# Performance work log

Hardware: AMD Instinct MI355X
Metric: run time of the kernel (lower is better)

The kernel has to match this reference:

```python
import jax, jax.numpy as jnp
import numpy as np

N_USERS = 100000
N_ITEMS = 50000
N_TOPICS = 1000
N_NODES = N_USERS + N_ITEMS + N_TOPICS
DIM = 64
LAYERS = 3
NNZ = 4000000
BATCH = 16384


def setup_inputs() -> dict:
    key = jax.random.key(0)
    ks = jax.random.split(key, 8)
    user_w = jax.random.normal(ks[0], (N_USERS, DIM), dtype=jnp.float32) * 0.1
    item_w = jax.random.normal(ks[1], (N_ITEMS, DIM), dtype=jnp.float32) * 0.1
    topic_w = jax.random.normal(ks[2], (N_TOPICS, DIM), dtype=jnp.float32) * 0.1
    vals = jax.random.uniform(ks[3], (NNZ,), dtype=jnp.float32)
    row = jax.random.randint(ks[4], (NNZ,), 0, N_NODES, dtype=jnp.int32)
    col = jax.random.randint(ks[5], (NNZ,), 0, N_NODES, dtype=jnp.int32)
    users = jax.random.randint(ks[6], (BATCH,), 0, N_USERS, dtype=jnp.int32)
    items = jax.random.randint(ks[7], (BATCH,), 0, N_ITEMS, dtype=jnp.int32)
    return {"user_w": user_w, "item_w": item_w, "topic_w": topic_w,
            "vals": vals, "row": row, "col": col,
            "users": users, "items": items}


def _spmm(vals, row, col, x):
    # y[r] = sum over edges e with row[e]==r of vals[e] * x[col[e]]
    msgs = vals[:, None] * x[col]  # [NNZ, DIM]
    return jax.ops.segment_sum(msgs, row, num_segments=N_NODES)


def reference(user_w, item_w, topic_w, vals, row, col, users, items):
    all_emb = jnp.concatenate([user_w, item_w, topic_w], axis=0)  # [N, D]
    acc = all_emb
    emb = all_emb
    for _ in range(LAYERS):
        emb = _spmm(vals, row, col, emb)
        acc = acc + emb
    out = acc / jnp.asarray(LAYERS + 1, dtype=acc.dtype)  # mean over stacked layers
    u = out[users]                       # [B, D] user rows
    i = out[N_USERS + items]             # [B, D] item rows (offset into node table)
    return jnp.sum(u * i, axis=1)        # [B]
```

## Files before the change

kernel.cpp:

```cpp
#include <hip/hip_runtime.h>
#include <hip/hip_fp16.h>

#define N_USERS 100000
#define N_ITEMS 50000
#define N_TOPICS 1000
#define N_NODES (N_USERS + N_ITEMS + N_TOPICS)
#define DIM 64
#define NNZ 4000000
#define BATCH 16384

#define BROWS 128
#define NB ((N_NODES + BROWS - 1) / BROWS)
#define NPART 256
#define CHUNK ((NNZ + NPART - 1) / NPART)
#define SEGCAP 4608

#define QSCALE 16384.0f
#define QINV   6.103515625e-05f

__global__ void concat_init(const float4* __restrict__ uw,
                            const float4* __restrict__ iw,
                            const float4* __restrict__ tw,
                            __half2* __restrict__ x0) {
    int tid = blockIdx.x * blockDim.x + threadIdx.x;
    const int total = N_NODES * (DIM / 4);
    if (tid >= total) return;
    int node = tid >> 4;
    int q = tid & 15;
    float4 v;
    if (node < N_USERS)                v = uw[node * 16 + q];
    else if (node < N_USERS + N_ITEMS) v = iw[(node - N_USERS) * 16 + q];
    else                               v = tw[(node - N_USERS - N_ITEMS) * 16 + q];
    x0[tid * 2]     = __floats2half2_rn(v.x, v.y);
    x0[tid * 2 + 1] = __floats2half2_rn(v.z, v.w);
}

__global__ void __launch_bounds__(1024)
part_count(const int* __restrict__ row, int* __restrict__ hcnt) {
    __shared__ int h[NB];
    const int g = blockIdx.x;
    const int t = threadIdx.x;
    for (int i = t; i < NB; i += 1024) h[i] = 0;
    __syncthreads();
    int e0 = g * CHUNK;
    int e1 = e0 + CHUNK; if (e1 > NNZ) e1 = NNZ;
    for (int e = e0 + t; e < e1; e += 1024) {
        int r = __builtin_nontemporal_load(&row[e]);
        atomicAdd(&h[r >> 7], 1);
    }
    __syncthreads();
    int* dst = hcnt + (size_t)g * NB;
    for (int i = t; i < NB; i += 1024) dst[i] = h[i];
}

__global__ void part_scanA(int* __restrict__ hcnt, int* __restrict__ bcnt) {
    int b = blockIdx.x * 4 + (threadIdx.x >> 6);
    int lane = threadIdx.x & 63;
    if (b >= NB) return;
    int carry = 0;
    for (int base = 0; base < NPART; base += 64) {
        int g = base + lane;
        int v = hcnt[(size_t)g * NB + b];
        int x = v;
        #pragma unroll
        for (int off = 1; off < 64; off <<= 1) {
            int y = __shfl_up(x, off, 64);
            if (lane >= off) x += y;
        }
        int tot = __shfl(x, 63, 64);
        hcnt[(size_t)g * NB + b] = carry + x - v;
        carry += tot;
    }
    if (lane == 0) bcnt[b] = carry;
}

__global__ void part_scanB(const int* __restrict__ bcnt,
                           int* __restrict__ bptr,
                           int* __restrict__ rowptr) {
    __shared__ int wsum[16];
    __shared__ int carry_s;
    const int t = threadIdx.x;
    const int lane = t & 63;
    const int wid = t >> 6;
    if (t == 0) carry_s = 0;
    __syncthreads();
    for (int base = 0; base < NB; base += 1024) {
        int i = base + t;
        int v = (i < NB) ? bcnt[i] : 0;
        int x = v;
        #pragma unroll
        for (int off = 1; off < 64; off <<= 1) {
            int y = __shfl_up(x, off, 64);
            if (lane >= off) x += y;
        }
        if (lane == 63) wsum[wid] = x;
        __syncthreads();
        int wbase = 0;
        for (int w = 0; w < wid; ++w) wbase += wsum[w];
        int excl = carry_s + wbase + (x - v);
        if (i < NB) bptr[i] = excl;
        __syncthreads();
        if (t == 1023) carry_s = excl + v;
        __syncthreads();
    }
    if (t == 0) { bptr[NB] = NNZ; rowptr[N_NODES] = NNZ; }
}

__global__ void __launch_bounds__(1024)
part_scatter(const int* __restrict__ row,
             const int* __restrict__ col,
             const float* __restrict__ vals,
             const int* __restrict__ hcnt,
             const int* __restrict__ bptr,
             int2* __restrict__ cvtmp) {
    __shared__ int cur[NB];
    const int g = blockIdx.x;
    const int t = threadIdx.x;
    const int* hoff = hcnt + (size_t)g * NB;
    for (int i = t; i < NB; i += 1024) cur[i] = bptr[i] + hoff[i];
    __syncthreads();
    int e0 = g * CHUNK;
    int e1 = e0 + CHUNK; if (e1 > NNZ) e1 = NNZ;
    for (int e = e0 + t; e < e1; e += 1024) {
        int r = __builtin_nontemporal_load(&row[e]);
        int c = __builtin_nontemporal_load(&col[e]);
        float v = __builtin_nontemporal_load(&vals[e]);
        int p = atomicAdd(&cur[r >> 7], 1);
        cvtmp[p] = make_int2(((r & (BROWS - 1)) << 18) | c, __float_as_int(v));
    }
}

__global__ void __launch_bounds__(256)
bucket_sort(const int* __restrict__ bptr,
            const long long* __restrict__ cvtmp,
            unsigned int* __restrict__ cv,
            int* __restrict__ rowptr) {
    __shared__ int2 seg[SEGCAP];
    __shared__ int cnt[BROWS];
    __shared__ int cur[BROWS];
    const int t = threadIdx.x;
    const int b = blockIdx.x;
    const int beg = bptr[b];
    const int end = bptr[b + 1];
    const int n = end - beg;

    for (int i = t; i < BROWS; i += 256) cnt[i] = 0;
    const bool lds_path = (n <= SEGCAP);

    if (lds_path) {
        for (int j = t; j < n; j += 256) {
            long long e = __builtin_nontemporal_load(&cvtmp[beg + j]);
            seg[j] = make_int2((int)e, (int)(e >> 32));
        }
    }
    __syncthreads();

    if (lds_path) {
        for (int j = t; j < n; j += 256)
            atomicAdd(&cnt[(seg[j].x >> 18) & (BROWS - 1)], 1);
    } else {
        for (int j = beg + t; j < end; j += 256) {
            long long e = cvtmp[j];
            atomicAdd(&cnt[((int)e >> 18) & (BROWS - 1)], 1);
        }
    }
    __syncthreads();

    if (t < 64) {
        int lane = t;
        int v0 = cnt[lane];
        int v1 = cnt[64 + lane];
        int x0 = v0;
        #pragma unroll
        for (int off = 1; off < 64; off <<= 1) {
            int y = __shfl_up(x0, off, 64);
            if (lane >= off) x0 += y;
        }
        int tot0 = __shfl(x0, 63, 64);
        int x1 = v1;
        #pragma unroll
        for (int off = 1; off < 64; off <<= 1) {
            int y = __shfl_up(x1, off, 64);
            if (lane >= off) x1 += y;
        }
        x1 += tot0;
        int e0 = x0 - v0;
        int e1 = x1 - v1;
        cur[lane] = e0;
        cur[64 + lane] = e1;
        int rowbase = b * BROWS;
        if (rowbase + lane < N_NODES)      rowptr[rowbase + lane] = beg + e0;
        if (rowbase + 64 + lane < N_NODES) rowptr[rowbase + 64 + lane] = beg + e1;
    }
    __syncthreads();

    if (lds_path) {
        for (int j = t; j < n; j += 256) {
            int2 e = seg[j];
            int p = atomicAdd(&cur[(e.x >> 18) & (BROWS - 1)], 1);
            float v = __int_as_float(e.y);
            unsigned int qv = (unsigned int)(v * QSCALE + 0.5f);
            if (qv > 16383u) qv = 16383u;
            cv[beg + p] = (qv << 18) | (unsigned int)(e.x & 0x3FFFF);
        }
    } else {
        for (int j = beg + t; j < end; j += 256) {
            long long e = cvtmp[j];
            int lo = (int)e;
            float v = __int_as_float((int)(e >> 32));
            int p = atomicAdd(&cur[(lo >> 18) & (BROWS - 1)], 1);
            unsigned int qv = (unsigned int)(v * QSCALE + 0.5f);
            if (qv > 16383u) qv = 16383u;
            cv[beg + p] = (qv << 18) | (unsigned int)(lo & 0x3FFFF);
        }
    }
}

__global__ void spmm_csr(const int* __restrict__ rowptr,
                         const unsigned int* __restrict__ cv,
                         const __half2* __restrict__ x2,
                         __half2* __restrict__ y2) {
    int blk = blockIdx.x;
    int bucket = (blk >> 8) * 8 + (blk & 7);
    int sub = (blk & 255) >> 3;
    int r = bucket * BROWS + sub * 4 + (threadIdx.x >> 6);
    if (r >= N_NODES) return;
    int lane = threadIdx.x & 63;
    int half = lane >> 5;
    int d = lane & 31;
    int beg = rowptr[r];
    int end = rowptr[r + 1];
    float ax0 = 0.0f, ay0 = 0.0f, ax1 = 0.0f, ay1 = 0.0f;
    int j = beg + half;
    for (; j + 14 < end; j += 16) {
        unsigned int u[8];
        __half2 h[8];
        #pragma unroll
        for (int k = 0; k < 8; ++k) u[k] = cv[j + 2 * k];
        #pragma unroll
        for (int k = 0; k < 8; ++k) h[k] = x2[(size_t)(u[k] & 0x3FFFF) * 32 + d];
        #pragma unroll
        for (int k = 0; k < 8; k += 2) {
            float2 f0 = __half22float2(h[k]);
            float2 f1 = __half22float2(h[k + 1]);
            float v0 = (float)(u[k] >> 18) * QINV;
            float v1 = (float)(u[k + 1] >> 18) * QINV;
            ax0 = fmaf(v0, f0.x, ax0); ay0 = fmaf(v0, f0.y, ay0);
            ax1 = fmaf(v1, f1.x, ax1); ay1 = fmaf(v1, f1.y, ay1);
        }
    }
    for (; j + 6 < end; j += 8) {
        unsigned int u0 = cv[j];
        unsigned int u1 = cv[j + 2];
        unsigned int u2 = cv[j + 4];
        unsigned int u3 = cv[j + 6];
        float2 f0 = __half22float2(x2[(size_t)(u0 & 0x3FFFF) * 32 + d]);
        float2 f1 = __half22float2(x2[(size_t)(u1 & 0x3FFFF) * 32 + d]);
        float2 f2 = __half22float2(x2[(size_t)(u2 & 0x3FFFF) * 32 + d]);
        float2 f3 = __half22float2(x2[(size_t)(u3 & 0x3FFFF) * 32 + d]);
        float v0 = (float)(u0 >> 18) * QINV;
        float v1 = (float)(u1 >> 18) * QINV;
        float v2 = (float)(u2 >> 18) * QINV;
        float v3 = (float)(u3 >> 18) * QINV;
        ax0 = fmaf(v0, f0.x, ax0); ay0 = fmaf(v0, f0.y, ay0);
        ax1 = fmaf(v1, f1.x, ax1); ay1 = fmaf(v1, f1.y, ay1);
        ax0 = fmaf(v2, f2.x, ax0); ay0 = fmaf(v2, f2.y, ay0);
        ax1 = fmaf(v3, f3.x, ax1); ay1 = fmaf(v3, f3.y, ay1);
    }
    for (; j < end; j += 2) {
        unsigned int u = cv[j];
        float2 f = __half22float2(x2[(size_t)(u & 0x3FFFF) * 32 + d]);
        float v = (float)(u >> 18) * QINV;
        ax0 = fmaf(v, f.x, ax0); ay0 = fmaf(v, f.y, ay0);
    }
    float ax = ax0 + ax1;
    float ay = ay0 + ay1;
    ax += __shfl_down(ax, 32, 64);
    ay += __shfl_down(ay, 32, 64);
    if (lane < 32) {
        __half2 o = __floats2half2_rn(ax, ay);
        unsigned int ob;
        __builtin_memcpy(&ob, &o, 4);
        __builtin_nontemporal_store(ob, (unsigned int*)&y2[(size_t)r * 32 + d]);
    }
}

__global__ void spmm_batch(const int* __restrict__ rowptr,
                           const unsigned int* __restrict__ cv,
                           const __half2* __restrict__ x2,
                           const int* __restrict__ users,
                           const int* __restrict__ items,
                           float* __restrict__ accb) {
    int b = blockIdx.x * 4 + (threadIdx.x >> 6);
    if (b >= 2 * BATCH) return;
    int lane = threadIdx.x & 63;
    int half = lane >> 5;
    int d = lane & 31;
    int r = (b < BATCH) ? users[b] : (N_USERS + items[b - BATCH]);
    int beg = rowptr[r];
    int end = rowptr[r + 1];
    float ax0 = 0.0f, ay0 = 0.0f, ax1 = 0.0f, ay1 = 0.0f;
    int j = beg + half;
    for (; j + 14 < end; j += 16) {
        unsigned int u[8];
        __half2 h[8];
        #pragma unroll
        for (int k = 0; k < 8; ++k) u[k] = cv[j + 2 * k];
        #pragma unroll
        for (int k = 0; k < 8; ++k) h[k] = x2[(size_t)(u[k] & 0x3FFFF) * 32 + d];
        #pragma unroll
        for (int k = 0; k < 8; k += 2) {
            float2 f0 = __half22float2(h[k]);
            float2 f1 = __half22float2(h[k + 1]);
            float v0 = (float)(u[k] >> 18) * QINV;
            float v1 = (float)(u[k + 1] >> 18) * QINV;
            ax0 = fmaf(v0, f0.x, ax0); ay0 = fmaf(v0, f0.y, ay0);
            ax1 = fmaf(v1, f1.x, ax1); ay1 = fmaf(v1, f1.y, ay1);
        }
    }
    for (; j + 6 < end; j += 8) {
        unsigned int u0 = cv[j];
        unsigned int u1 = cv[j + 2];
        unsigned int u2 = cv[j + 4];
        unsigned int u3 = cv[j + 6];
        float2 f0 = __half22float2(x2[(size_t)(u0 & 0x3FFFF) * 32 + d]);
        float2 f1 = __half22float2(x2[(size_t)(u1 & 0x3FFFF) * 32 + d]);
        float2 f2 = __half22float2(x2[(size_t)(u2 & 0x3FFFF) * 32 + d]);
        float2 f3 = __half22float2(x2[(size_t)(u3 & 0x3FFFF) * 32 + d]);
        float v0 = (float)(u0 >> 18) * QINV;
        float v1 = (float)(u1 >> 18) * QINV;
        float v2 = (float)(u2 >> 18) * QINV;
        float v3 = (float)(u3 >> 18) * QINV;
        ax0 = fmaf(v0, f0.x, ax0); ay0 = fmaf(v0, f0.y, ay0);
        ax1 = fmaf(v1, f1.x, ax1); ay1 = fmaf(v1, f1.y, ay1);
        ax0 = fmaf(v2, f2.x, ax0); ay0 = fmaf(v2, f2.y, ay0);
        ax1 = fmaf(v3, f3.x, ax1); ay1 = fmaf(v3, f3.y, ay1);
    }
    for (; j < end; j += 2) {
        unsigned int u = cv[j];
        float2 f = __half22float2(x2[(size_t)(u & 0x3FFFF) * 32 + d]);
        float v = (float)(u >> 18) * QINV;
        ax0 = fmaf(v, f.x, ax0); ay0 = fmaf(v, f.y, ay0);
    }
    float ax = ax0 + ax1;
    float ay = ay0 + ay1;
    ax += __shfl_down(ax, 32, 64);
    ay += __shfl_down(ay, 32, 64);
    if (lane < 32) {
        float2* a2 = (float2*)(accb + (size_t)b * 64 + 2 * d);
        float2 o = *a2;
        o.x += ax; o.y += ay;
        *a2 = o;
    }
}

__global__ void batch_init(const float4* __restrict__ uw,
                           const float4* __restrict__ iw,
                           const int* __restrict__ users,
                           const int* __restrict__ items,
                           float4* __restrict__ accb) {
    int tid = blockIdx.x * blockDim.x + threadIdx.x;
    const int total = 2 * BATCH * (DIM / 4);
    if (tid >= total) return;
    int r = tid >> 4;
    int q = tid & 15;
    float4 v;
    if (r < BATCH) v = uw[(size_t)users[r] * 16 + q];
    else           v = iw[(size_t)items[r - BATCH] * 16 + q];
    accb[tid] = v;
}

__global__ void batch_add(const __half* __restrict__ emb,
                          const int* __restrict__ users,
                          const int* __restrict__ items,
                          float4* __restrict__ accb) {
    int tid = blockIdx.x * blockDim.x + threadIdx.x;
    const int total = 2 * BATCH * (DIM / 4);
    if (tid >= total) return;
    int r = tid >> 4;
    int q = tid & 15;
    int node = (r < BATCH) ? users[r] : (N_USERS + items[r - BATCH]);
    const __half2* e2 = (const __half2*)(emb + (size_t)node * 64 + q * 4);
    float2 lo = __half22float2(e2[0]);
    float2 hi = __half22float2(e2[1]);
    float4 a = accb[tid];
    a.x += lo.x; a.y += lo.y; a.z += hi.x; a.w += hi.y;
    accb[tid] = a;
}

__global__ void final_dot(const float* __restrict__ accb,
                          float* __restrict__ out) {
    int b = blockIdx.x * 4 + (threadIdx.x >> 6);
    int lane = threadIdx.x & 63;
    if (b >= BATCH) return;
    float pu = accb[(size_t)b * 64 + lane];
    float pi = accb[(size_t)(BATCH + b) * 64 + lane];
    float p = pu * pi;
    #pragma unroll
    for (int off = 32; off > 0; off >>= 1)
        p += __shfl_down(p, off, 64);
    if (lane == 0) out[b] = p * (1.0f / 16.0f);
}

extern "C" void kernel_launch(void* const* d_in, const int* in_sizes, int n_in,
                              void* d_out, int out_size, void* d_ws, size_t ws_size,
                              hipStream_t stream) {
    const float* uw   = (const float*)d_in[0];
    const float* iw   = (const float*)d_in[1];
    const float* tw   = (const float*)d_in[2];
    const float* vals = (const float*)d_in[3];
    const int*   row  = (const int*)d_in[4];
    const int*   col  = (const int*)d_in[5];
    const int*   users= (const int*)d_in[6];
    const int*   items= (const int*)d_in[7];
    float* out = (float*)d_out;

    char* ws = (char*)d_ws;
    const size_t NODE_F = (size_t)N_NODES * DIM;
    __half* A     = (__half*)ws; ws += NODE_F * 2;
    __half* B     = (__half*)ws; ws += NODE_F * 2;
    float* ACCB   = (float*)ws;  ws += (size_t)2 * BATCH * DIM * 4;
    int*   bcnt   = (int*)ws;    ws += (size_t)NB * 4;
    int*   bptr   = (int*)ws;    ws += (size_t)(NB + 1) * 4;
    int*   rowptr = (int*)ws;    ws += (size_t)(N_NODES + 1) * 4;
    int*   hcnt   = (int*)ws;    ws += (size_t)NPART * NB * 4;
    unsigned int* cv = (unsigned int*)ws; ws += (size_t)NNZ * 4;
    int2*  cvtmp  = (int2*)ws;   ws += (size_t)NNZ * 8;

    const int node_v4  = N_NODES * (DIM / 4);
    const int batch_v4 = 2 * BATCH * (DIM / 4);

    concat_init<<<(node_v4 + 255) / 256, 256, 0, stream>>>(
        (const float4*)uw, (const float4*)iw, (const float4*)tw, (__half2*)A);
    batch_init<<<(batch_v4 + 255) / 256, 256, 0, stream>>>(
        (const float4*)uw, (const float4*)iw, users, items, (float4*)ACCB);

    part_count<<<NPART, 1024, 0, stream>>>(row, hcnt);
    part_scanA<<<(NB + 3) / 4, 256, 0, stream>>>(hcnt, bcnt);
    part_scanB<<<1, 1024, 0, stream>>>(bcnt, bptr, rowptr);
    part_scatter<<<NPART, 1024, 0, stream>>>(row, col, vals, hcnt, bptr, cvtmp);
    bucket_sort<<<NB, 256, 0, stream>>>(bptr, (const long long*)cvtmp, cv, rowptr);

    const int spmm_blocks = ((NB + 7) / 8) * 256;
    spmm_csr<<<spmm_blocks, 256, 0, stream>>>(rowptr, cv, (const __half2*)A,
                                              (__half2*)B);
    batch_add<<<(batch_v4 + 255) / 256, 256, 0, stream>>>(
        B, users, items, (float4*)ACCB);
    spmm_csr<<<spmm_blocks, 256, 0, stream>>>(rowptr, cv, (const __half2*)B,
                                              (__half2*)A);
    batch_add<<<(batch_v4 + 255) / 256, 256, 0, stream>>>(
        A, users, items, (float4*)ACCB);
    spmm_batch<<<(2 * BATCH + 3) / 4, 256, 0, stream>>>(
        rowptr, cv, (const __half2*)A, users, items, ACCB);

    final_dot<<<(BATCH + 3) / 4, 256, 0, stream>>>(ACCB, out);
}
```

Before: 442.7 us.

## Fuse setup kernels and map one SpMM row per half-wavefront

Merges concat, batch init and partition counting into one launch, and folds the two scan kernels into one using a last-block atomic counter. The SpMM kernels now assign each 32-lane half-wave its own row instead of splitting a row's edges across the two halves. This removes the cross-half shuffle reduction and reduces launch overhead. In exchange, each row's edges are processed serially by one half-wave, which lengthens per-row dependency chains and increases load imbalance on long rows.

```diff
diff --git a/kernel.cpp b/kernel.cpp
--- a/kernel.cpp
+++ b/kernel.cpp
@@ -18,45 +18,71 @@
 #define QSCALE 16384.0f
 #define QINV   6.103515625e-05f
 
-__global__ void concat_init(const float4* __restrict__ uw,
-                            const float4* __restrict__ iw,
-                            const float4* __restrict__ tw,
-                            __half2* __restrict__ x0) {
-    int tid = blockIdx.x * blockDim.x + threadIdx.x;
-    const int total = N_NODES * (DIM / 4);
-    if (tid >= total) return;
-    int node = tid >> 4;
-    int q = tid & 15;
-    float4 v;
-    if (node < N_USERS)                v = uw[node * 16 + q];
-    else if (node < N_USERS + N_ITEMS) v = iw[(node - N_USERS) * 16 + q];
-    else                               v = tw[(node - N_USERS - N_ITEMS) * 16 + q];
-    x0[tid * 2]     = __floats2half2_rn(v.x, v.y);
-    x0[tid * 2 + 1] = __floats2half2_rn(v.z, v.w);
-}
+#define CONCAT_TOTAL (N_NODES * (DIM / 4))
+#define CONCAT_BLOCKS ((CONCAT_TOTAL + 1023) / 1024)
+#define BINIT_TOTAL (2 * BATCH * (DIM / 4))
+#define BINIT_BLOCKS ((BINIT_TOTAL + 1023) / 1024)
 
 __global__ void __launch_bounds__(1024)
-part_count(const int* __restrict__ row, int* __restrict__ hcnt) {
+phase0(const float4* __restrict__ uw,
+       const float4* __restrict__ iw,
+       const float4* __restrict__ tw,
+       const int* __restrict__ row,
+       const int* __restrict__ users,
+       const int* __restrict__ items,
+       __half2* __restrict__ x0,
+       float4* __restrict__ accb,
+       int* __restrict__ hcnt,
+       int* __restrict__ sync) {
     __shared__ int h[NB];
-    const int g = blockIdx.x;
+    const int blk = blockIdx.x;
     const int t = threadIdx.x;
-    for (int i = t; i < NB; i += 1024) h[i] = 0;
-    __syncthreads();
-    int e0 = g * CHUNK;
-    int e1 = e0 + CHUNK; if (e1 > NNZ) e1 = NNZ;
-    for (int e = e0 + t; e < e1; e += 1024) {
-        int r = __builtin_nontemporal_load(&row[e]);
-        atomicAdd(&h[r >> 7], 1);
-    }
-    __syncthreads();
-    int* dst = hcnt + (size_t)g * NB;
-    for (int i = t; i < NB; i += 1024) dst[i] = h[i];
-}
-
-__global__ void part_scanA(int* __restrict__ hcnt, int* __restrict__ bcnt) {
-    int b = blockIdx.x * 4 + (threadIdx.x >> 6);
-    int lane = threadIdx.x & 63;
-    if (b >= NB) return;
+    if (blk < NPART) {
+        if (blk == 0 && t == 0) *sync = 0;
+        for (int i = t; i < NB; i += 1024) h[i] = 0;
+        __syncthreads();
+        int e0 = blk * CHUNK;
+        int e1 = e0 + CHUNK; if (e1 > NNZ) e1 = NNZ;
+        for (int e = e0 + t; e < e1; e += 1024) {
+            int r = __builtin_nontemporal_load(&row[e]);
+            atomicAdd(&h[r >> 7], 1);
+        }
+        __syncthreads();
+        int* dst = hcnt + (size_t)blk * NB;
+        for (int i = t; i < NB; i += 1024) dst[i] = h[i];
+    } else if (blk < NPART + CONCAT_BLOCKS) {
+        int tid = (blk - NPART) * 1024 + t;
+        if (tid >= CONCAT_TOTAL) return;
+        int node = tid >> 4;
+        int q = tid & 15;
+        float4 v;
+        if (node < N_USERS)                v = uw[node * 16 + q];
+        else if (node < N_USERS + N_ITEMS) v = iw[(node - N_USERS) * 16 + q];
+        else                               v = tw[(node - N_USERS - N_ITEMS) * 16 + q];
+        x0[tid * 2]     = __floats2half2_rn(v.x, v.y);
+        x0[tid * 2 + 1] = __floats2half2_rn(v.z, v.w);
+    } else {
+        int tid = (blk - NPART - CONCAT_BLOCKS) * 1024 + t;
+        if (tid >= BINIT_TOTAL) return;
+        int r = tid >> 4;
+        int q = tid & 15;
+        float4 v;
+        if (r < BATCH) v = uw[(size_t)users[r] * 16 + q];
+        else           v = iw[(size_t)items[r - BATCH] * 16 + q];
+        accb[tid] = v;
+    }
+}
+
+__global__ void __launch_bounds__(256)
+part_scanAB(int* __restrict__ hcnt,
+            int* __restrict__ bcnt,
+            int* __restrict__ bptr,
+            int* __restrict__ rowptr,
+            int* __restrict__ sync) {
+    const int t = threadIdx.x;
+    const int lane = t & 63;
+    const int wid = t >> 6;
+    int b = blockIdx.x * 4 + wid;
     int carry = 0;
     for (int base = 0; base < NPART; base += 64) {
         int g = base + lane;
@@ -72,19 +98,18 @@
         carry += tot;
     }
     if (lane == 0) bcnt[b] = carry;
-}
-
-__global__ void part_scanB(const int* __restrict__ bcnt,
-                           int* __restrict__ bptr,
-                           int* __restrict__ rowptr) {
-    __shared__ int wsum[16];
+    __syncthreads();
+    __threadfence();
+    __shared__ int lastFlag;
+    if (t == 0) lastFlag = (atomicAdd(sync, 1) == (int)gridDim.x - 1);
+    __syncthreads();
+    if (!lastFlag) return;
+
+    __shared__ int wsum[4];
     __shared__ int carry_s;
-    const int t = threadIdx.x;
-    const int lane = t & 63;
-    const int wid = t >> 6;
     if (t == 0) carry_s = 0;
     __syncthreads();
-    for (int base = 0; base < NB; base += 1024) {
+    for (int base = 0; base < NB; base += 256) {
         int i = base + t;
         int v = (i < NB) ? bcnt[i] : 0;
         int x = v;
@@ -100,7 +125,7 @@
         int excl = carry_s + wbase + (x - v);
         if (i < NB) bptr[i] = excl;
         __syncthreads();
-        if (t == 1023) carry_s = excl + v;
+        if (t == 255) carry_s = excl + v;
         __syncthreads();
     }
     if (t == 0) { bptr[NB] = NNZ; rowptr[N_NODES] = NNZ; }
@@ -220,69 +245,69 @@
                          const unsigned int* __restrict__ cv,
                          const __half2* __restrict__ x2,
                          __half2* __restrict__ y2) {
-    int blk = blockIdx.x;
-    int bucket = (blk >> 8) * 8 + (blk & 7);
-    int sub = (blk & 255) >> 3;
-    int r = bucket * BROWS + sub * 4 + (threadIdx.x >> 6);
-    if (r >= N_NODES) return;
+    int bucket = blockIdx.x >> 4;
+    int sub = blockIdx.x & 15;
     int lane = threadIdx.x & 63;
     int half = lane >> 5;
+    int r = bucket * BROWS + sub * 8 + (threadIdx.x >> 6) * 2 + half;
+    if (r >= N_NODES) return;
     int d = lane & 31;
     int beg = rowptr[r];
     int end = rowptr[r + 1];
-    float ax0 = 0.0f, ay0 = 0.0f, ax1 = 0.0f, ay1 = 0.0f;
-    int j = beg + half;
-    for (; j + 14 < end; j += 16) {
+    float ax = 0.0f, ay = 0.0f;
+    int j = beg;
+    for (; j + 15 < end; j += 16) {
+        unsigned int u[16];
+        __half2 h[16];
+        #pragma unroll
+        for (int k = 0; k < 16; ++k) u[k] = cv[j + k];
+        #pragma unroll
+        for (int k = 0; k < 16; ++k) h[k] = x2[(size_t)(u[k] & 0x3FFFF) * 32 + d];
+        #pragma unroll
+        for (int k = 0; k < 16; ++k) {
+            float2 f = __half22float2(h[k]);
+            float v = (float)(u[k] >> 18) * QINV;
+            ax = fmaf(v, f.x, ax); ay = fmaf(v, f.y, ay);
+        }
+    }
+    for (; j + 7 < end; j += 8) {
         unsigned int u[8];
         __half2 h[8];
         #pragma unroll
-        for (int k = 0; k < 8; ++k) u[k] = cv[j + 2 * k];
+        for (int k = 0; k < 8; ++k) u[k] = cv[j + k];
         #pragma unroll
         for (int k = 0; k < 8; ++k) h[k] = x2[(size_t)(u[k] & 0x3FFFF) * 32 + d];
         #pragma unroll
-        for (int k = 0; k < 8; k += 2) {
-            float2 f0 = __half22float2(h[k]);
-            float2 f1 = __half22float2(h[k + 1]);
-            float v0 = (float)(u[k] >> 18) * QINV;
-            float v1 = (float)(u[k + 1] >> 18) * QINV;
-            ax0 = fmaf(v0, f0.x, ax0); ay0 = fmaf(v0, f0.y, ay0);
-            ax1 = fmaf(v1, f1.x, ax1); ay1 = fmaf(v1, f1.y, ay1);
-        }
-    }
-    for (; j + 6 < end; j += 8) {
-        unsigned int u0 = cv[j];
-        unsigned int u1 = cv[j + 2];
-        unsigned int u2 = cv[j + 4];
-        unsigned int u3 = cv[j + 6];
-        float2 f0 = __half22float2(x2[(size_t)(u0 & 0x3FFFF) * 32 + d]);
-        float2 f1 = __half22float2(x2[(size_t)(u1 & 0x3FFFF) * 32 + d]);
-        float2 f2 = __half22float2(x2[(size_t)(u2 & 0x3FFFF) * 32 + d]);
-        float2 f3 = __half22float2(x2[(size_t)(u3 & 0x3FFFF) * 32 + d]);
-        float v0 = (float)(u0 >> 18) * QINV;
-        float v1 = (float)(u1 >> 18) * QINV;
-        float v2 = (float)(u2 >> 18) * QINV;
-        float v3 = (float)(u3 >> 18) * QINV;
-        ax0 = fmaf(v0, f0.x, ax0); ay0 = fmaf(v0, f0.y, ay0);
-        ax1 = fmaf(v1, f1.x, ax1); ay1 = fmaf(v1, f1.y, ay1);
-        ax0 = fmaf(v2, f2.x, ax0); ay0 = fmaf(v2, f2.y, ay0);
-        ax1 = fmaf(v3, f3.x, ax1); ay1 = fmaf(v3, f3.y, ay1);
-    }
-    for (; j < end; j += 2) {
+        for (int k = 0; k < 8; ++k) {
+            float2 f = __half22float2(h[k]);
+            float v = (float)(u[k] >> 18) * QINV;
+            ax = fmaf(v, f.x, ax); ay = fmaf(v, f.y, ay);
+        }
+    }
+    for (; j + 3 < end; j += 4) {
+        unsigned int u[4];
+        __half2 h[4];
+        #pragma unroll
+        for (int k = 0; k < 4; ++k) u[k] = cv[j + k];
+        #pragma unroll
+        for (int k = 0; k < 4; ++k) h[k] = x2[(size_t)(u[k] & 0x3FFFF) * 32 + d];
+        #pragma unroll
+        for (int k = 0; k < 4; ++k) {
+            float2 f = __half22float2(h[k]);
+            float v = (float)(u[k] >> 18) * QINV;
+            ax = fmaf(v, f.x, ax); ay = fmaf(v, f.y, ay);
+        }
+    }
+    for (; j < end; ++j) {
         unsigned int u = cv[j];
         float2 f = __half22float2(x2[(size_t)(u & 0x3FFFF) * 32 + d]);
         float v = (float)(u >> 18) * QINV;
-        ax0 = fmaf(v, f.x, ax0); ay0 = fmaf(v, f.y, ay0);
-    }
-    float ax = ax0 + ax1;
-    float ay = ay0 + ay1;
-    ax += __shfl_down(ax, 32, 64);
-    ay += __shfl_down(ay, 32, 64);
-    if (lane < 32) {
-        __half2 o = __floats2half2_rn(ax, ay);
-        unsigned int ob;
-        __builtin_memcpy(&ob, &o, 4);
-        __builtin_nontemporal_store(ob, (unsigned int*)&y2[(size_t)r * 32 + d]);
-    }
+        ax = fmaf(v, f.x, ax); ay = fmaf(v, f.y, ay);
+    }
+    __half2 o = __floats2half2_rn(ax, ay);
+    unsigned int ob;
+    __builtin_memcpy(&ob, &o, 4);
+    __builtin_nontemporal_store(ob, (unsigned int*)&y2[(size_t)r * 32 + d]);
 }
 
 __global__ void spmm_batch(const int* __restrict__ rowptr,
@@ -291,83 +316,68 @@
                            const int* __restrict__ users,
                            const int* __restrict__ items,
                            float* __restrict__ accb) {
-    int b = blockIdx.x * 4 + (threadIdx.x >> 6);
-    if (b >= 2 * BATCH) return;
     int lane = threadIdx.x & 63;
     int half = lane >> 5;
+    int b = blockIdx.x * 8 + (threadIdx.x >> 6) * 2 + half;
+    if (b >= 2 * BATCH) return;
     int d = lane & 31;
     int r = (b < BATCH) ? users[b] : (N_USERS + items[b - BATCH]);
     int beg = rowptr[r];
     int end = rowptr[r + 1];
-    float ax0 = 0.0f, ay0 = 0.0f, ax1 = 0.0f, ay1 = 0.0f;
-    int j = beg + half;
-    for (; j + 14 < end; j += 16) {
+    float ax = 0.0f, ay = 0.0f;
+    int j = beg;
+    for (; j + 15 < end; j += 16) {
+        unsigned int u[16];
+        __half2 h[16];
+        #pragma unroll
+        for (int k = 0; k < 16; ++k) u[k] = cv[j + k];
+        #pragma unroll
+        for (int k = 0; k < 16; ++k) h[k] = x2[(size_t)(u[k] & 0x3FFFF) * 32 + d];
+        #pragma unroll
+        for (int k = 0; k < 16; ++k) {
+            float2 f = __half22float2(h[k]);
+            float v = (float)(u[k] >> 18) * QINV;
+            ax = fmaf(v, f.x, ax); ay = fmaf(v, f.y, ay);
+        }
+    }
+    for (; j + 7 < end; j += 8) {
         unsigned int u[8];
         __half2 h[8];
         #pragma unroll
-        for (int k = 0; k < 8; ++k) u[k] = cv[j + 2 * k];
+        for (int k = 0; k < 8; ++k) u[k] = cv[j + k];
         #pragma unroll
         for (int k = 0; k < 8; ++k) h[k] = x2[(size_t)(u[k] & 0x3FFFF) * 32 + d];
         #pragma unroll
-        for (int k = 0; k < 8; k += 2) {
-            float2 f0 = __half22float2(h[k]);
-            float2 f1 = __half22float2(h[k + 1]);
-            float v0 = (float)(u[k] >> 18) * QINV;
-            float v1 = (float)(u[k + 1] >> 18) * QINV;
-            ax0 = fmaf(v0, f0.x, ax0); ay0 = fmaf(v0, f0.y, ay0);
-            ax1 = fmaf(v1, f1.x, ax1); ay1 = fmaf(v1, f1.y, ay1);
-        }
-    }
-    for (; j + 6 < end; j += 8) {
-        unsigned int u0 = cv[j];
-        unsigned int u1 = cv[j + 2];
-        unsigned int u2 = cv[j + 4];
-        unsigned int u3 = cv[j + 6];
-        float2 f0 = __half22float2(x2[(size_t)(u0 & 0x3FFFF) * 32 + d]);
-        float2 f1 = __half22float2(x2[(size_t)(u1 & 0x3FFFF) * 32 + d]);
-        float2 f2 = __half22float2(x2[(size_t)(u2 & 0x3FFFF) * 32 + d]);
-        float2 f3 = __half22float2(x2[(size_t)(u3 & 0x3FFFF) * 32 + d]);
-        float v0 = (float)(u0 >> 18) * QINV;
-        float v1 = (float)(u1 >> 18) * QINV;
-        float v2 = (float)(u2 >> 18) * QINV;
-        float v3 = (float)(u3 >> 18) * QINV;
-        ax0 = fmaf(v0, f0.x, ax0); ay0 = fmaf(v0, f0.y, ay0);
-        ax1 = fmaf(v1, f1.x, ax1); ay1 = fmaf(v1, f1.y, ay1);
-        ax0 = fmaf(v2, f2.x, ax0); ay0 = fmaf(v2, f2.y, ay0);
-        ax1 = fmaf(v3, f3.x, ax1); ay1 = fmaf(v3, f3.y, ay1);
-    }
-    for (; j < end; j += 2) {
+        for (int k = 0; k < 8; ++k) {
+            float2 f = __half22float2(h[k]);
+            float v = (float)(u[k] >> 18) * QINV;
+            ax = fmaf(v, f.x, ax); ay = fmaf(v, f.y, ay);
+        }
+    }
+    for (; j + 3 < end; j += 4) {
+        unsigned int u[4];
+        __half2 h[4];
+        #pragma unroll
+        for (int k = 0; k < 4; ++k) u[k] = cv[j + k];
+        #pragma unroll
+        for (int k = 0; k < 4; ++k) h[k] = x2[(size_t)(u[k] & 0x3FFFF) * 32 + d];
+        #pragma unroll
+        for (int k = 0; k < 4; ++k) {
+            float2 f = __half22float2(h[k]);
+            float v = (float)(u[k] >> 18) * QINV;
+            ax = fmaf(v, f.x, ax); ay = fmaf(v, f.y, ay);
+        }
+    }
+    for (; j < end; ++j) {
         unsigned int u = cv[j];
         float2 f = __half22float2(x2[(size_t)(u & 0x3FFFF) * 32 + d]);
         float v = (float)(u >> 18) * QINV;
-        ax0 = fmaf(v, f.x, ax0); ay0 = fmaf(v, f.y, ay0);
-    }
-    float ax = ax0 + ax1;
-    float ay = ay0 + ay1;
-    ax += __shfl_down(ax, 32, 64);
-    ay += __shfl_down(ay, 32, 64);
-    if (lane < 32) {
-        float2* a2 = (float2*)(accb + (size_t)b * 64 + 2 * d);
-        float2 o = *a2;
-        o.x += ax; o.y += ay;
-        *a2 = o;
-    }
-}
-
-__global__ void batch_init(const float4* __restrict__ uw,
-                           const float4* __restrict__ iw,
-                           const int* __restrict__ users,
-                           const int* __restrict__ items,
-                           float4* __restrict__ accb) {
-    int tid = blockIdx.x * blockDim.x + threadIdx.x;
-    const int total = 2 * BATCH * (DIM / 4);
-    if (tid >= total) return;
-    int r = tid >> 4;
-    int q = tid & 15;
-    float4 v;
-    if (r < BATCH) v = uw[(size_t)users[r] * 16 + q];
-    else           v = iw[(size_t)items[r - BATCH] * 16 + q];
-    accb[tid] = v;
+        ax = fmaf(v, f.x, ax); ay = fmaf(v, f.y, ay);
+    }
+    float2* a2 = (float2*)(accb + (size_t)b * 64 + 2 * d);
+    float2 o = *a2;
+    o.x += ax; o.y += ay;
+    *a2 = o;
 }
 
 __global__ void batch_add(const __half* __restrict__ emb,
@@ -424,24 +434,21 @@
     int*   bptr   = (int*)ws;    ws += (size_t)(NB + 1) * 4;
     int*   rowptr = (int*)ws;    ws += (size_t)(N_NODES + 1) * 4;
     int*   hcnt   = (int*)ws;    ws += (size_t)NPART * NB * 4;
+    int*   sync   = (int*)ws;    ws += 64;
     unsigned int* cv = (unsigned int*)ws; ws += (size_t)NNZ * 4;
     int2*  cvtmp  = (int2*)ws;   ws += (size_t)NNZ * 8;
 
-    const int node_v4  = N_NODES * (DIM / 4);
     const int batch_v4 = 2 * BATCH * (DIM / 4);
 
-    concat_init<<<(node_v4 + 255) / 256, 256, 0, stream>>>(
-        (const float4*)uw, (const float4*)iw, (const float4*)tw, (__half2*)A);
-    batch_init<<<(batch_v4 + 255) / 256, 256, 0, stream>>>(
-        (const float4*)uw, (const float4*)iw, users, items, (float4*)ACCB);
-
-    part_count<<<NPART, 1024, 0, stream>>>(row, hcnt);
-    part_scanA<<<(NB + 3) / 4, 256, 0, stream>>>(hcnt, bcnt);
-    part_scanB<<<1, 1024, 0, stream>>>(bcnt, bptr, rowptr);
+    phase0<<<NPART + CONCAT_BLOCKS + BINIT_BLOCKS, 1024, 0, stream>>>(
+        (const float4*)uw, (const float4*)iw, (const float4*)tw, row,
+        users, items, (__half2*)A, (float4*)ACCB, hcnt, sync);
+
+    part_scanAB<<<NB / 4, 256, 0, stream>>>(hcnt, bcnt, bptr, rowptr, sync);
     part_scatter<<<NPART, 1024, 0, stream>>>(row, col, vals, hcnt, bptr, cvtmp);
     bucket_sort<<<NB, 256, 0, stream>>>(bptr, (const long long*)cvtmp, cv, rowptr);
 
-    const int spmm_blocks = ((NB + 7) / 8) * 256;
+    const int spmm_blocks = NB * 16;
     spmm_csr<<<spmm_blocks, 256, 0, stream>>>(rowptr, cv, (const __half2*)A,
                                               (__half2*)B);
     batch_add<<<(batch_v4 + 255) / 256, 256, 0, stream>>>(
@@ -450,7 +457,7 @@
                                               (__half2*)A);
     batch_add<<<(batch_v4 + 255) / 256, 256, 0, stream>>>(
         A, users, items, (float4*)ACCB);
-    spmm_batch<<<(2 * BATCH + 3) / 4, 256, 0, stream>>>(
+    spmm_batch<<<(2 * BATCH + 7) / 8, 256, 0, stream>>>(
         rowptr, cv, (const __half2*)A, users, items, ACCB);
 
     final_dot<<<(BATCH + 3) / 4, 256, 0, stream>>>(ACCB, out);
```

Result: no change. 446.3 us (+0.8%).
